# Optimization experiments

Hardware: AMD Instinct MI355X
Metric: run time of the kernel (lower is better)

## Reference

```python
import jax, jax.numpy as jnp
import numpy as np

DIM = 768
HEADS = 12
DIM_HEAD = 64
INNER = HEADS * DIM_HEAD  # 768
SCALE = DIM_HEAD ** -0.5
LN_EPS = 1e-5


def setup_inputs() -> dict:
    key = jax.random.key(0)
    ks = jax.random.split(key, 6)
    B, N = 2, 1024
    x = jax.random.normal(ks[0], (B, N, DIM), dtype=jnp.float32)
    ln_g = jnp.ones((DIM,), jnp.float32)
    ln_b = jnp.zeros((DIM,), jnp.float32)
    # torch nn.Linear weights are [out, in]
    w_qkv = jax.random.normal(ks[1], (3 * INNER, DIM), jnp.float32) * (DIM ** -0.5)
    w_out = jax.random.normal(ks[2], (DIM, INNER), jnp.float32) * (INNER ** -0.5)
    b_out = jnp.zeros((DIM,), jnp.float32)
    theta = jax.random.normal(ks[3], (HEADS, HEADS), jnp.float32)
    # xavier_uniform for 12x12
    lim = float(np.sqrt(6.0 / (HEADS + HEADS)))
    gnn_w = jax.random.uniform(ks[4], (HEADS, HEADS), jnp.float32, -lim, lim)
    return {"x": x, "ln_g": ln_g, "ln_b": ln_b, "w_qkv": w_qkv,
            "w_out": w_out, "b_out": b_out, "theta": theta, "gnn_w": gnn_w}


def _dc_crd(attn, theta, gnn_w):
    # attn: [B, H, N, N] treated as image with H=12 channels
    B, H, N, _ = attn.shape
    w = attn.mean(axis=(-2, -1))  # adaptive_avg_pool2d -> [B, H]
    diff = w[:, :, None] - w[:, None, :]  # [B, H, H]
    # abs(1 - exp(-d)/(1+exp(-d))) - 1 == abs(1 - sigmoid(-d)) - 1
    T_w = jnp.abs(1.0 - jax.nn.sigmoid(-diff)) - 1.0
    adj = (T_w + jnp.swapaxes(T_w, -1, -2)) * 0.5 * theta  # [B, H, H]
    attn_flat = attn.reshape(B, H, N * N)
    support = jnp.einsum('ij,bjm->bim', gnn_w, attn_flat)  # W @ features
    out = jax.nn.relu(jnp.einsum('bij,bjm->bim', adj, support))  # spmm(adj, support)
    return out.reshape(B, H, N, N)


def reference(x, ln_g, ln_b, w_qkv, w_out, b_out, theta, gnn_w):
    B, N, D = x.shape
    mu = x.mean(-1, keepdims=True)
    var = x.var(-1, keepdims=True)
    xn = (x - mu) * jax.lax.rsqrt(var + LN_EPS) * ln_g + ln_b
    qkv = xn @ w_qkv.T  # [B, N, 3*INNER]
    q, k, v = jnp.split(qkv, 3, axis=-1)
    def heads(t):
        return t.reshape(B, N, HEADS, DIM_HEAD).transpose(0, 2, 1, 3)
    q, k, v = heads(q), heads(k), heads(v)  # [B, H, N, d]
    dots = jnp.einsum('bhnd,bhmd->bhnm', q, k) * SCALE
    attn = jax.nn.softmax(dots, axis=-1)
    H = _dc_crd(attn, theta, gnn_w)
    out = jnp.einsum('bhnm,bhmd->bhnd', attn + H, v)
    out = out.transpose(0, 2, 1, 3).reshape(B, N, INNER)
    return out @ w_out.T + b_out
```

## Files before the change

kernel.cpp:

```cpp
#include <hip/hip_runtime.h>
#include <hip/hip_bf16.h>
#include <stdint.h>

#define NB 2
#define SEQ 1024
#define DMODEL 768
#define NH 12
#define DH 64
#define SCALE 0.125f
#define NCH 4

#define AJ_RS 1288
#define CT_HS 648

typedef __hip_bfloat16 bf16;
typedef __attribute__((ext_vector_type(8))) short short8;
typedef __attribute__((ext_vector_type(2))) short s2v;
typedef __attribute__((ext_vector_type(4))) float f32x4;

__device__ __forceinline__ bf16 f2b(float x){ return __float2bfloat16(x); }
__device__ __forceinline__ short f2bs(float x){
  bf16 h = __float2bfloat16(x); return *reinterpret_cast<short*>(&h);
}
__device__ __forceinline__ float s2f(short u){
  return __uint_as_float(((unsigned)(unsigned short)u) << 16);
}

__device__ __forceinline__ void gl_lds16(const bf16* g, bf16* l){
  __builtin_amdgcn_global_load_lds(
      (const __attribute__((address_space(1))) void*)g,
      (__attribute__((address_space(3))) void*)l, 16, 0, 0);
}

__global__ __launch_bounds__(256) void prep_all(const float* __restrict__ x,
                                                const float* __restrict__ g,
                                                const float* __restrict__ bta,
                                                const float* __restrict__ w1, int n1,
                                                const float* __restrict__ w2, int n2,
                                                const float* __restrict__ theta,
                                                const float* __restrict__ gnn,
                                                bf16* __restrict__ xn,
                                                bf16* __restrict__ wb,
                                                bf16* __restrict__ Mb,
                                                float* __restrict__ l){
  int bx = blockIdx.x, t = threadIdx.x;
  if (bx < 2048){
    const float* xr = x + (size_t)bx*DMODEL;
    float v0[3]; float s = 0.f, s2 = 0.f;
    #pragma unroll
    for (int i=0;i<3;i++){ float val = xr[t+256*i]; v0[i]=val; s+=val; s2+=val*val; }
    __shared__ float sb[256], s2b[256];
    sb[t]=s; s2b[t]=s2; __syncthreads();
    for (int off=128; off>0; off>>=1){
      if (t<off){ sb[t]+=sb[t+off]; s2b[t]+=s2b[t+off]; }
      __syncthreads();
    }
    float mean = sb[0]*(1.f/DMODEL);
    float var  = s2b[0]*(1.f/DMODEL) - mean*mean;
    float rstd = rsqrtf(var + 1e-5f);
    #pragma unroll
    for (int i=0;i<3;i++){
      int c = t+256*i;
      xn[(size_t)bx*DMODEL + c] = f2b((v0[i]-mean)*rstd*g[c] + bta[c]);
    }
  } else if (bx < 2048+9216){
    int i = (bx-2048)*256 + t;
    if (i < n1) wb[i] = f2b(w1[i]);
    else if (i < n1+n2) wb[i] = f2b(w2[i-n1]);
  } else {
    int sub = bx - (2048+9216);
    if (sub == 0){
      #pragma unroll
      for (int e=0;e<2;e++){
        int idx = t + 256*e;
        int i = idx >> 5, j = idx & 31;
        float sacc = 0.f;
        if (i < 12 && j < 12)
          for (int jj=0;jj<12;jj++) sacc += (-0.5f)*theta[i*12+jj] * gnn[jj*12+j];
        bf16 hi = f2b(sacc);
        float lo = sacc - __bfloat162float(hi);
        Mb[idx]       = hi;
        Mb[512 + idx] = f2b(lo);
      }
    } else {
      l[(sub-1)*256 + t] = 0.f;
    }
  }
}

__global__ __launch_bounds__(256) void gemm_qkv(const bf16* __restrict__ A,
                                                const bf16* __restrict__ W,
                                                bf16* __restrict__ q,
                                                bf16* __restrict__ k,
                                                bf16* __restrict__ vt){
  __shared__ bf16 As[128*32];
  __shared__ bf16 Bs[128*32];
  int n0 = blockIdx.x*128, m0 = blockIdx.y*128;
  int t = threadIdx.x, w = t>>6, lane = t&63;
  int ln16 = lane&15, q8 = (lane>>4)*8;
  int wm = w>>1, wn = w&1;
  f32x4 acc[4][4] = {};
  for (int k0=0; k0<768; k0+=32){
    __syncthreads();
    #pragma unroll
    for (int i=0;i<2;i++){
      int cc = t + i*256;
      int r = cc>>2, ko = (cc&3)*8;
      gl_lds16(&A[(size_t)(m0+r)*768 + k0+ko], &As[(size_t)(w*64 + i*256)*8]);
      gl_lds16(&W[(size_t)(n0+r)*768 + k0+ko], &Bs[(size_t)(w*64 + i*256)*8]);
    }
    __syncthreads();
    short8 af[4], bfr[4];
    #pragma unroll
    for (int mi=0;mi<4;mi++) af[mi]  = *(const short8*)&As[(wm*64+mi*16+ln16)*32 + q8];
    #pragma unroll
    for (int ni=0;ni<4;ni++) bfr[ni] = *(const short8*)&Bs[(wn*64+ni*16+ln16)*32 + q8];
    #pragma unroll
    for (int mi=0;mi<4;mi++)
      #pragma unroll
      for (int ni=0;ni<4;ni++)
        acc[mi][ni] = __builtin_amdgcn_mfma_f32_16x16x32_bf16(af[mi], bfr[ni], acc[mi][ni], 0, 0, 0);
  }
  int quad4 = (lane>>4)*4;
  #pragma unroll
  for (int mi=0;mi<4;mi++){
    #pragma unroll
    for (int ni=0;ni<4;ni++){
      int cg = n0 + wn*64 + ni*16 + ln16;
      int which = cg/768; int rem = cg - which*768;
      int h = rem>>6, dd = rem&63;
      #pragma unroll
      for (int r=0;r<4;r++){
        int m = m0 + wm*64 + mi*16 + quad4 + r;
        int bb = m>>10, n = m&1023;
        float val = acc[mi][ni][r];
        if (which==0)      q [((size_t)(bb*NH+h)*SEQ + n)*DH + dd] = f2b(val*SCALE);
        else if (which==1) k [((size_t)(bb*NH+h)*SEQ + n)*DH + dd] = f2b(val);
        else               vt[((size_t)(bb*NH+h)*DH + dd)*SEQ + n] = f2b(val);
      }
    }
  }
}

__global__ __launch_bounds__(768) void attn_sums(const bf16* __restrict__ q,
                                                 const bf16* __restrict__ k,
                                                 float* __restrict__ l){
  int b = blockIdx.z, ch = blockIdx.y; int r0 = blockIdx.x*16;
  int t = threadIdx.x; int h = t>>6; int lane = t&63;
  int ln16 = lane&15, quad = lane>>4; int q8 = quad*8, quad4 = quad*4;
  const bf16* qrow = q + ((size_t)(b*NH+h)*SEQ + r0 + ln16)*DH;
  short8 aq0 = *(const short8*)(qrow + q8);
  short8 aq1 = *(const short8*)(qrow + 32 + q8);
  const bf16* kB = k + ((size_t)(b*NH+h)*SEQ)*DH;
  float ls[4] = {0.f,0.f,0.f,0.f};
  #pragma unroll 4
  for (int i=0;i<16;i++){
    int c0 = ch*256 + i*16;
    const bf16* krow = kB + (size_t)(c0 + ln16)*DH;
    short8 bk0 = *(const short8*)(krow + q8);
    short8 bk1 = *(const short8*)(krow + 32 + q8);
    f32x4 a = {0.f,0.f,0.f,0.f};
    a = __builtin_amdgcn_mfma_f32_16x16x32_bf16(aq0, bk0, a, 0, 0, 0);
    a = __builtin_amdgcn_mfma_f32_16x16x32_bf16(aq1, bk1, a, 0, 0, 0);
    #pragma unroll
    for (int r=0;r<4;r++) ls[r] += __expf(a[r]);
  }
  #pragma unroll
  for (int msk=1; msk<16; msk<<=1){
    #pragma unroll
    for (int r=0;r<4;r++) ls[r] += __shfl_xor(ls[r], msk);
  }
  if (ln16 == 0){
    #pragma unroll
    for (int r=0;r<4;r++)
      atomicAdd(&l[((size_t)(b*NH+h))*SEQ + r0 + quad4 + r], ls[r]);
  }
}

__global__ __launch_bounds__(768) void attn_main(const bf16* __restrict__ q,
                                                 const bf16* __restrict__ k,
                                                 const bf16* __restrict__ vt,
                                                 const bf16* __restrict__ Mb,
                                                 const float* __restrict__ l,
                                                 bf16* __restrict__ opart){
  __shared__ __align__(16) bf16 attJ[16*AJ_RS];
  __shared__ __align__(16) bf16 combT[16*CT_HS];
  int b = blockIdx.z, ch = blockIdx.y; int r0 = blockIdx.x*16;
  int t = threadIdx.x; int h = t>>6; int lane = t&63;
  int ln16 = lane&15, quad = lane>>4; int q8 = quad*8, quad4 = quad*4;
  const bf16* kB = k  + ((size_t)(b*NH+h)*SEQ)*DH;
  const bf16* vB = vt + ((size_t)(b*NH+h)*DH)*SEQ;

  short8 z8 = (short8){0,0,0,0,0,0,0,0};
  for (int i = t*8; i < 16*AJ_RS; i += 768*8) *(short8*)&attJ[i] = z8;

  short8 mhi = *(const short8*)&Mb[ln16*32 + q8];
  short8 mlo = *(const short8*)&Mb[512 + ln16*32 + q8];

  const bf16* qrow = q + ((size_t)(b*NH+h)*SEQ + r0 + ln16)*DH;
  short8 aq0 = *(const short8*)(qrow + q8);
  short8 aq1 = *(const short8*)(qrow + 32 + q8);

  float inv_l[4];
  #pragma unroll
  for (int r=0;r<4;r++) inv_l[r] = 1.0f / l[((size_t)(b*NH+h))*SEQ + r0 + quad4 + r];

  __syncthreads();

  f32x4 oacc[4] = {};
  for (int it=0; it<8; it++){
    int c0 = ch*256 + it*32;
    #pragma unroll
    for (int half=0; half<2; half++){
      const bf16* krow = kB + (size_t)(c0 + half*16 + ln16)*DH;
      short8 bk0 = *(const short8*)(krow + q8);
      short8 bk1 = *(const short8*)(krow + 32 + q8);
      f32x4 a = {0.f,0.f,0.f,0.f};
      a = __builtin_amdgcn_mfma_f32_16x16x32_bf16(aq0, bk0, a, 0, 0, 0);
      a = __builtin_amdgcn_mfma_f32_16x16x32_bf16(aq1, bk1, a, 0, 0, 0);
      int cc = half*16 + ln16;
      #pragma unroll
      for (int r=0;r<4;r++)
        attJ[(quad4+r)*AJ_RS + cc*40 + h] = f2b(__expf(a[r])*inv_l[r]);
    }
    __syncthreads();
    for (int tl = h; tl < 32; tl += 12){
      int n = tl*16 + ln16;
      int base = (n>>5)*AJ_RS + (n&31)*40;
      short8 bfrag = *(const short8*)&attJ[base + q8];
      f32x4 c = {0.f,0.f,0.f,0.f};
      c = __builtin_amdgcn_mfma_f32_16x16x32_bf16(mlo, bfrag, c, 0, 0, 0);
      c = __builtin_amdgcn_mfma_f32_16x16x32_bf16(mhi, bfrag, c, 0, 0, 0);
      s2v id01 = *(const s2v*)&attJ[base + quad4];
      s2v id23 = *(const s2v*)&attJ[base + quad4 + 2];
      float idf[4] = { s2f(id01[0]), s2f(id01[1]), s2f(id23[0]), s2f(id23[1]) };
      int cbase = (n>>5)*40 + (n&31);
      #pragma unroll
      for (int ri=0; ri<4; ri++)
        combT[(quad4+ri)*CT_HS + cbase] = f2b(idf[ri] + fmaxf(c[ri], 0.f));
    }
    __syncthreads();
    short8 afrag = *(const short8*)&combT[h*CT_HS + ln16*40 + q8];
    #pragma unroll
    for (int ni=0; ni<4; ni++){
      short8 bv = *(const short8*)&vB[(size_t)(ni*16 + ln16)*SEQ + c0 + q8];
      oacc[ni] = __builtin_amdgcn_mfma_f32_16x16x32_bf16(afrag, bv, oacc[ni], 0, 0, 0);
    }
  }
  bf16* dst = opart + ((size_t)ch*NB*SEQ + (size_t)b*SEQ)*DMODEL;
  #pragma unroll
  for (int ni=0; ni<4; ni++)
    #pragma unroll
    for (int r=0; r<4; r++){
      int n = r0 + quad4 + r;
      dst[(size_t)n*DMODEL + h*DH + ni*16 + ln16] = f2b(oacc[ni][r]);
    }
}

__global__ __launch_bounds__(256) void reduce_kernel(const bf16* __restrict__ opart,
                                                     bf16* __restrict__ aout){
  const size_t TOT = (size_t)NB*SEQ*DMODEL;
  size_t i = ((size_t)blockIdx.x*256 + threadIdx.x)*8;
  float s[8] = {};
  #pragma unroll
  for (int c=0;c<NCH;c++){
    short8 u = *(const short8*)&opart[c*TOT + i];
    #pragma unroll
    for (int e=0;e<8;e++) s[e] += s2f(u[e]);
  }
  short8 o;
  #pragma unroll
  for (int e=0;e<8;e++) o[e] = f2bs(s[e]);
  *(short8*)&aout[i] = o;
}

__global__ __launch_bounds__(256) void gemm_out(const bf16* __restrict__ A,
                                                const bf16* __restrict__ W,
                                                const float* __restrict__ bias,
                                                float* __restrict__ out){
  __shared__ bf16 As[64*32];
  __shared__ bf16 Bs[64*32];
  int n0 = blockIdx.x*64, m0 = blockIdx.y*64;
  int t = threadIdx.x, w = t>>6, lane = t&63;
  int ln16 = lane&15, q8 = (lane>>4)*8;
  int wm = w>>1, wn = w&1;
  f32x4 acc[2][2] = {};
  for (int k0=0; k0<768; k0+=32){
    __syncthreads();
    {
      int r = t>>2, ko = (t&3)*8;
      gl_lds16(&A[(size_t)(m0+r)*768 + k0+ko], &As[(size_t)(w*64)*8]);
      gl_lds16(&W[(size_t)(n0+r)*768 + k0+ko], &Bs[(size_t)(w*64)*8]);
    }
    __syncthreads();
    short8 af[2], bfr[2];
    #pragma unroll
    for (int mi=0;mi<2;mi++) af[mi]  = *(const short8*)&As[(wm*32+mi*16+ln16)*32 + q8];
    #pragma unroll
    for (int ni=0;ni<2;ni++) bfr[ni] = *(const short8*)&Bs[(wn*32+ni*16+ln16)*32 + q8];
    #pragma unroll
    for (int mi=0;mi<2;mi++)
      #pragma unroll
      for (int ni=0;ni<2;ni++)
        acc[mi][ni] = __builtin_amdgcn_mfma_f32_16x16x32_bf16(af[mi], bfr[ni], acc[mi][ni], 0, 0, 0);
  }
  int quad4 = (lane>>4)*4;
  #pragma unroll
  for (int mi=0;mi<2;mi++)
    #pragma unroll
    for (int ni=0;ni<2;ni++){
      int cg = n0 + wn*32 + ni*16 + ln16;
      #pragma unroll
      for (int r=0;r<4;r++){
        int m = m0 + wm*32 + mi*16 + quad4 + r;
        out[(size_t)m*768 + cg] = acc[mi][ni][r] + bias[cg];
      }
    }
}

extern "C" void kernel_launch(void* const* d_in, const int* in_sizes, int n_in,
                              void* d_out, int out_size, void* d_ws, size_t ws_size,
                              hipStream_t stream){
  const float* x     = (const float*)d_in[0];
  const float* ln_g  = (const float*)d_in[1];
  const float* ln_b  = (const float*)d_in[2];
  const float* w_qkv = (const float*)d_in[3];
  const float* w_out = (const float*)d_in[4];
  const float* b_out = (const float*)d_in[5];
  const float* theta = (const float*)d_in[6];
  const float* gnn   = (const float*)d_in[7];
  float* out = (float*)d_out;

  char* p = (char*)d_ws;
  bf16* xnb   = (bf16*)p; p += (size_t)2048*768*2;
  bf16* wqkvb = (bf16*)p; p += (size_t)2304*768*2;
  bf16* woutb = (bf16*)p; p += (size_t)768*768*2;
  bf16* qb    = (bf16*)p; p += (size_t)NB*NH*SEQ*DH*2;
  bf16* kb    = (bf16*)p; p += (size_t)NB*NH*SEQ*DH*2;
  bf16* vtb   = (bf16*)p; p += (size_t)NB*NH*SEQ*DH*2;
  bf16* aoutb = (bf16*)p; p += (size_t)2048*768*2;
  bf16* Mbw   = (bf16*)p; p += (size_t)1024*2;
  float* lsum = (float*)p; p += (size_t)NB*NH*SEQ*4;
  bf16* opart = (bf16*)p;

  const int N1 = 2304*768, N2 = 768*768;
  prep_all<<<dim3(2048+9216+97), dim3(256), 0, stream>>>(
      x, ln_g, ln_b, w_qkv, N1, w_out, N2, theta, gnn, xnb, wqkvb, Mbw, lsum);
  gemm_qkv<<<dim3(18, 16), dim3(256), 0, stream>>>(xnb, wqkvb, qb, kb, vtb);
  attn_sums<<<dim3(64, NCH, NB), dim3(768), 0, stream>>>(qb, kb, lsum);
  attn_main<<<dim3(64, NCH, NB), dim3(768), 0, stream>>>(qb, kb, vtb, Mbw, lsum, opart);
  reduce_kernel<<<dim3(NB*SEQ*DMODEL/(8*256)), dim3(256), 0, stream>>>(opart, aoutb);
  gemm_out<<<dim3(12, 32), dim3(256), 0, stream>>>(aoutb, woutb, b_out, out);
}
```

Measured before the change: 202.0 us.

## Fuse attention row-sum and main attention kernels with inter-block spin barrier

Merges the softmax-denominator kernel and the main attention kernel into one launch. Each block computes its partial row sums, atomically adds them, then spins on a per-row-block counter until all NCH column-chunk blocks have contributed, and reads the totals back through atomics. This removes one kernel launch and keeps the Q fragments and setup in registers across both phases. It relies on all four chunk blocks of a row group being co-resident, which risks deadlock or stalls, and the spin-wait adds latency.

```diff
diff --git a/kernel.cpp b/kernel.cpp
--- a/kernel.cpp
+++ b/kernel.cpp
@@ -42,7 +42,8 @@
                                                 bf16* __restrict__ xn,
                                                 bf16* __restrict__ wb,
                                                 bf16* __restrict__ Mb,
-                                                float* __restrict__ l){
+                                                float* __restrict__ l,
+                                                unsigned* __restrict__ cnt){
   int bx = blockIdx.x, t = threadIdx.x;
   if (bx < 2048){
     const float* xr = x + (size_t)bx*DMODEL;
@@ -82,8 +83,10 @@
         Mb[idx]       = hi;
         Mb[512 + idx] = f2b(lo);
       }
+    } else if (sub <= 96){
+      l[(sub-1)*256 + t] = 0.f;
     } else {
-      l[(sub-1)*256 + t] = 0.f;
+      if (t < 128) cnt[t] = 0u;
     }
   }
 }
@@ -142,16 +145,31 @@
   }
 }
 
-__global__ __launch_bounds__(768) void attn_sums(const bf16* __restrict__ q,
-                                                 const bf16* __restrict__ k,
-                                                 float* __restrict__ l){
+__global__ __launch_bounds__(768) void attn_fused(const bf16* __restrict__ q,
+                                                  const bf16* __restrict__ k,
+                                                  const bf16* __restrict__ vt,
+                                                  const bf16* __restrict__ Mb,
+                                                  float* __restrict__ l,
+                                                  unsigned* __restrict__ cnt,
+                                                  bf16* __restrict__ opart){
+  __shared__ __align__(16) bf16 attJ[16*AJ_RS];
+  __shared__ __align__(16) bf16 combT[16*CT_HS];
   int b = blockIdx.z, ch = blockIdx.y; int r0 = blockIdx.x*16;
   int t = threadIdx.x; int h = t>>6; int lane = t&63;
   int ln16 = lane&15, quad = lane>>4; int q8 = quad*8, quad4 = quad*4;
+  const bf16* kB = k  + ((size_t)(b*NH+h)*SEQ)*DH;
+  const bf16* vB = vt + ((size_t)(b*NH+h)*DH)*SEQ;
+
+  short8 z8 = (short8){0,0,0,0,0,0,0,0};
+  for (int i = t*8; i < 16*AJ_RS; i += 768*8) *(short8*)&attJ[i] = z8;
+
+  short8 mhi = *(const short8*)&Mb[ln16*32 + q8];
+  short8 mlo = *(const short8*)&Mb[512 + ln16*32 + q8];
+
   const bf16* qrow = q + ((size_t)(b*NH+h)*SEQ + r0 + ln16)*DH;
   short8 aq0 = *(const short8*)(qrow + q8);
   short8 aq1 = *(const short8*)(qrow + 32 + q8);
-  const bf16* kB = k + ((size_t)(b*NH+h)*SEQ)*DH;
+
   float ls[4] = {0.f,0.f,0.f,0.f};
   #pragma unroll 4
   for (int i=0;i<16;i++){
@@ -170,42 +188,27 @@
     #pragma unroll
     for (int r=0;r<4;r++) ls[r] += __shfl_xor(ls[r], msk);
   }
+  size_t lbase = ((size_t)(b*NH+h))*SEQ + r0 + quad4;
   if (ln16 == 0){
     #pragma unroll
-    for (int r=0;r<4;r++)
-      atomicAdd(&l[((size_t)(b*NH+h))*SEQ + r0 + quad4 + r], ls[r]);
-  }
-}
-
-__global__ __launch_bounds__(768) void attn_main(const bf16* __restrict__ q,
-                                                 const bf16* __restrict__ k,
-                                                 const bf16* __restrict__ vt,
-                                                 const bf16* __restrict__ Mb,
-                                                 const float* __restrict__ l,
-                                                 bf16* __restrict__ opart){
-  __shared__ __align__(16) bf16 attJ[16*AJ_RS];
-  __shared__ __align__(16) bf16 combT[16*CT_HS];
-  int b = blockIdx.z, ch = blockIdx.y; int r0 = blockIdx.x*16;
-  int t = threadIdx.x; int h = t>>6; int lane = t&63;
-  int ln16 = lane&15, quad = lane>>4; int q8 = quad*8, quad4 = quad*4;
-  const bf16* kB = k  + ((size_t)(b*NH+h)*SEQ)*DH;
-  const bf16* vB = vt + ((size_t)(b*NH+h)*DH)*SEQ;
-
-  short8 z8 = (short8){0,0,0,0,0,0,0,0};
-  for (int i = t*8; i < 16*AJ_RS; i += 768*8) *(short8*)&attJ[i] = z8;
-
-  short8 mhi = *(const short8*)&Mb[ln16*32 + q8];
-  short8 mlo = *(const short8*)&Mb[512 + ln16*32 + q8];
-
-  const bf16* qrow = q + ((size_t)(b*NH+h)*SEQ + r0 + ln16)*DH;
-  short8 aq0 = *(const short8*)(qrow + q8);
-  short8 aq1 = *(const short8*)(qrow + 32 + q8);
-
+    for (int r=0;r<4;r++) atomicAdd(&l[lbase + r], ls[r]);
+  }
+
+  __threadfence();
+  __syncthreads();
+  int gidx = b*64 + blockIdx.x;
+  if (t == 0){
+    atomicAdd(&cnt[gidx], 1u);
+    while (atomicAdd(&cnt[gidx], 0u) < NCH) __builtin_amdgcn_s_sleep(2);
+  }
+  __syncthreads();
+
+  float lv[4];
+  #pragma unroll
+  for (int r=0;r<4;r++) lv[r] = (ln16 == 0) ? atomicAdd(&l[lbase + r], 0.0f) : 0.f;
   float inv_l[4];
   #pragma unroll
-  for (int r=0;r<4;r++) inv_l[r] = 1.0f / l[((size_t)(b*NH+h))*SEQ + r0 + quad4 + r];
-
-  __syncthreads();
+  for (int r=0;r<4;r++) inv_l[r] = 1.0f / __shfl(lv[r], quad*16);
 
   f32x4 oacc[4] = {};
   for (int it=0; it<8; it++){
@@ -285,13 +288,11 @@
   int ln16 = lane&15, q8 = (lane>>4)*8;
   int wm = w>>1, wn = w&1;
   f32x4 acc[2][2] = {};
+  int r = t>>2, ko = (t&3)*8;
   for (int k0=0; k0<768; k0+=32){
     __syncthreads();
-    {
-      int r = t>>2, ko = (t&3)*8;
-      gl_lds16(&A[(size_t)(m0+r)*768 + k0+ko], &As[(size_t)(w*64)*8]);
-      gl_lds16(&W[(size_t)(n0+r)*768 + k0+ko], &Bs[(size_t)(w*64)*8]);
-    }
+    gl_lds16(&A[(size_t)(m0+r)*768 + k0+ko], &As[(size_t)(w*64)*8]);
+    gl_lds16(&W[(size_t)(n0+r)*768 + k0+ko], &Bs[(size_t)(w*64)*8]);
     __syncthreads();
     short8 af[2], bfr[2];
     #pragma unroll
@@ -311,9 +312,9 @@
     for (int ni=0;ni<2;ni++){
       int cg = n0 + wn*32 + ni*16 + ln16;
       #pragma unroll
-      for (int r=0;r<4;r++){
-        int m = m0 + wm*32 + mi*16 + quad4 + r;
-        out[(size_t)m*768 + cg] = acc[mi][ni][r] + bias[cg];
+      for (int rr=0;rr<4;rr++){
+        int m = m0 + wm*32 + mi*16 + quad4 + rr;
+        out[(size_t)m*768 + cg] = acc[mi][ni][rr] + bias[cg];
       }
     }
 }
@@ -341,14 +342,14 @@
   bf16* aoutb = (bf16*)p; p += (size_t)2048*768*2;
   bf16* Mbw   = (bf16*)p; p += (size_t)1024*2;
   float* lsum = (float*)p; p += (size_t)NB*NH*SEQ*4;
+  unsigned* cntw = (unsigned*)p; p += (size_t)128*4;
   bf16* opart = (bf16*)p;
 
   const int N1 = 2304*768, N2 = 768*768;
-  prep_all<<<dim3(2048+9216+97), dim3(256), 0, stream>>>(
-      x, ln_g, ln_b, w_qkv, N1, w_out, N2, theta, gnn, xnb, wqkvb, Mbw, lsum);
+  prep_all<<<dim3(2048+9216+98), dim3(256), 0, stream>>>(
+      x, ln_g, ln_b, w_qkv, N1, w_out, N2, theta, gnn, xnb, wqkvb, Mbw, lsum, cntw);
   gemm_qkv<<<dim3(18, 16), dim3(256), 0, stream>>>(xnb, wqkvb, qb, kb, vtb);
-  attn_sums<<<dim3(64, NCH, NB), dim3(768), 0, stream>>>(qb, kb, lsum);
-  attn_main<<<dim3(64, NCH, NB), dim3(768), 0, stream>>>(qb, kb, vtb, Mbw, lsum, opart);
+  attn_fused<<<dim3(64, NCH, NB), dim3(768), 0, stream>>>(qb, kb, vtb, Mbw, lsum, cntw, opart);
   reduce_kernel<<<dim3(NB*SEQ*DMODEL/(8*256)), dim3(256), 0, stream>>>(opart, aoutb);
   gemm_out<<<dim3(12, 32), dim3(256), 0, stream>>>(aoutb, woutb, b_out, out);
 }
```

Result: slower. 319.7 us (+58.3%).

## Store unnormalized exp scores in attn_sums, reuse in attn_main, fuse reduce into gemm_out

Applied to the files above, without the earlier changes.

attn_sums now writes the bf16 exp(QK) values it computes to a workspace buffer. attn_main reads them back, prefetching the next iteration, instead of recomputing the QK MFMAs and exps. The separate reduce kernel is removed: gemm_out sums the NCH partial outputs while loading its A tile. This trades recomputation for about 50MB of extra global traffic (NB*NH*SEQ*SEQ*2 bytes written and read), and it adds an extra bf16 rounding before normalization.

```diff
diff --git a/kernel.cpp b/kernel.cpp
--- a/kernel.cpp
+++ b/kernel.cpp
@@ -17,6 +17,7 @@
 typedef __attribute__((ext_vector_type(8))) short short8;
 typedef __attribute__((ext_vector_type(2))) short s2v;
 typedef __attribute__((ext_vector_type(4))) float f32x4;
+typedef unsigned long long u64;
 
 __device__ __forceinline__ bf16 f2b(float x){ return __float2bfloat16(x); }
 __device__ __forceinline__ short f2bs(float x){
@@ -144,14 +145,16 @@
 
 __global__ __launch_bounds__(768) void attn_sums(const bf16* __restrict__ q,
                                                  const bf16* __restrict__ k,
-                                                 float* __restrict__ l){
-  int b = blockIdx.z, ch = blockIdx.y; int r0 = blockIdx.x*16;
+                                                 float* __restrict__ l,
+                                                 u64* __restrict__ pst){
+  int rg = blockIdx.x, ch = blockIdx.y, b = blockIdx.z; int r0 = rg*16;
   int t = threadIdx.x; int h = t>>6; int lane = t&63;
   int ln16 = lane&15, quad = lane>>4; int q8 = quad*8, quad4 = quad*4;
   const bf16* qrow = q + ((size_t)(b*NH+h)*SEQ + r0 + ln16)*DH;
   short8 aq0 = *(const short8*)(qrow + q8);
   short8 aq1 = *(const short8*)(qrow + 32 + q8);
   const bf16* kB = k + ((size_t)(b*NH+h)*SEQ)*DH;
+  u64* pb = pst + ((((size_t)(b*NCH+ch)*64 + rg)*NH + h)*16)*64 + lane;
   float ls[4] = {0.f,0.f,0.f,0.f};
   #pragma unroll 4
   for (int i=0;i<16;i++){
@@ -162,8 +165,11 @@
     f32x4 a = {0.f,0.f,0.f,0.f};
     a = __builtin_amdgcn_mfma_f32_16x16x32_bf16(aq0, bk0, a, 0, 0, 0);
     a = __builtin_amdgcn_mfma_f32_16x16x32_bf16(aq1, bk1, a, 0, 0, 0);
-    #pragma unroll
-    for (int r=0;r<4;r++) ls[r] += __expf(a[r]);
+    float e0 = __expf(a[0]), e1 = __expf(a[1]), e2 = __expf(a[2]), e3 = __expf(a[3]);
+    ls[0]+=e0; ls[1]+=e1; ls[2]+=e2; ls[3]+=e3;
+    unsigned p0 = ((unsigned)(unsigned short)f2bs(e1) << 16) | (unsigned)(unsigned short)f2bs(e0);
+    unsigned p1 = ((unsigned)(unsigned short)f2bs(e3) << 16) | (unsigned)(unsigned short)f2bs(e2);
+    pb[(size_t)i*64] = ((u64)p1 << 32) | (u64)p0;
   }
   #pragma unroll
   for (int msk=1; msk<16; msk<<=1){
@@ -177,19 +183,18 @@
   }
 }
 
-__global__ __launch_bounds__(768) void attn_main(const bf16* __restrict__ q,
-                                                 const bf16* __restrict__ k,
-                                                 const bf16* __restrict__ vt,
-                                                 const bf16* __restrict__ Mb,
-                                                 const float* __restrict__ l,
-                                                 bf16* __restrict__ opart){
+__global__ __launch_bounds__(768, 6) void attn_main(const bf16* __restrict__ vt,
+                                                    const bf16* __restrict__ Mb,
+                                                    const float* __restrict__ l,
+                                                    const u64* __restrict__ pst,
+                                                    bf16* __restrict__ opart){
   __shared__ __align__(16) bf16 attJ[16*AJ_RS];
   __shared__ __align__(16) bf16 combT[16*CT_HS];
-  int b = blockIdx.z, ch = blockIdx.y; int r0 = blockIdx.x*16;
+  int rg = blockIdx.x, ch = blockIdx.y, b = blockIdx.z; int r0 = rg*16;
   int t = threadIdx.x; int h = t>>6; int lane = t&63;
   int ln16 = lane&15, quad = lane>>4; int q8 = quad*8, quad4 = quad*4;
-  const bf16* kB = k  + ((size_t)(b*NH+h)*SEQ)*DH;
   const bf16* vB = vt + ((size_t)(b*NH+h)*DH)*SEQ;
+  const u64* pb = pst + ((((size_t)(b*NCH+ch)*64 + rg)*NH + h)*16)*64 + lane;
 
   short8 z8 = (short8){0,0,0,0,0,0,0,0};
   for (int i = t*8; i < 16*AJ_RS; i += 768*8) *(short8*)&attJ[i] = z8;
@@ -197,31 +202,28 @@
   short8 mhi = *(const short8*)&Mb[ln16*32 + q8];
   short8 mlo = *(const short8*)&Mb[512 + ln16*32 + q8];
 
-  const bf16* qrow = q + ((size_t)(b*NH+h)*SEQ + r0 + ln16)*DH;
-  short8 aq0 = *(const short8*)(qrow + q8);
-  short8 aq1 = *(const short8*)(qrow + 32 + q8);
-
   float inv_l[4];
   #pragma unroll
   for (int r=0;r<4;r++) inv_l[r] = 1.0f / l[((size_t)(b*NH+h))*SEQ + r0 + quad4 + r];
+
+  u64 cur0 = pb[0*64], cur1 = pb[1*64];
 
   __syncthreads();
 
   f32x4 oacc[4] = {};
   for (int it=0; it<8; it++){
     int c0 = ch*256 + it*32;
+    int nx = (it+1)&7;
+    u64 n0 = pb[(size_t)(nx*2+0)*64], n1 = pb[(size_t)(nx*2+1)*64];
     #pragma unroll
     for (int half=0; half<2; half++){
-      const bf16* krow = kB + (size_t)(c0 + half*16 + ln16)*DH;
-      short8 bk0 = *(const short8*)(krow + q8);
-      short8 bk1 = *(const short8*)(krow + 32 + q8);
-      f32x4 a = {0.f,0.f,0.f,0.f};
-      a = __builtin_amdgcn_mfma_f32_16x16x32_bf16(aq0, bk0, a, 0, 0, 0);
-      a = __builtin_amdgcn_mfma_f32_16x16x32_bf16(aq1, bk1, a, 0, 0, 0);
       int cc = half*16 + ln16;
-      #pragma unroll
-      for (int r=0;r<4;r++)
-        attJ[(quad4+r)*AJ_RS + cc*40 + h] = f2b(__expf(a[r])*inv_l[r]);
+      u64 cu = half ? cur1 : cur0;
+      unsigned p0 = (unsigned)cu, p1 = (unsigned)(cu >> 32);
+      attJ[(quad4+0)*AJ_RS + cc*40 + h] = f2b(s2f((short)(p0 & 0xffff))*inv_l[0]);
+      attJ[(quad4+1)*AJ_RS + cc*40 + h] = f2b(s2f((short)(p0 >> 16))   *inv_l[1]);
+      attJ[(quad4+2)*AJ_RS + cc*40 + h] = f2b(s2f((short)(p1 & 0xffff))*inv_l[2]);
+      attJ[(quad4+3)*AJ_RS + cc*40 + h] = f2b(s2f((short)(p1 >> 16))   *inv_l[3]);
     }
     __syncthreads();
     for (int tl = h; tl < 32; tl += 12){
@@ -246,6 +248,7 @@
       short8 bv = *(const short8*)&vB[(size_t)(ni*16 + ln16)*SEQ + c0 + q8];
       oacc[ni] = __builtin_amdgcn_mfma_f32_16x16x32_bf16(afrag, bv, oacc[ni], 0, 0, 0);
     }
+    cur0 = n0; cur1 = n1;
   }
   bf16* dst = opart + ((size_t)ch*NB*SEQ + (size_t)b*SEQ)*DMODEL;
   #pragma unroll
@@ -257,41 +260,33 @@
     }
 }
 
-__global__ __launch_bounds__(256) void reduce_kernel(const bf16* __restrict__ opart,
-                                                     bf16* __restrict__ aout){
-  const size_t TOT = (size_t)NB*SEQ*DMODEL;
-  size_t i = ((size_t)blockIdx.x*256 + threadIdx.x)*8;
-  float s[8] = {};
-  #pragma unroll
-  for (int c=0;c<NCH;c++){
-    short8 u = *(const short8*)&opart[c*TOT + i];
-    #pragma unroll
-    for (int e=0;e<8;e++) s[e] += s2f(u[e]);
-  }
-  short8 o;
-  #pragma unroll
-  for (int e=0;e<8;e++) o[e] = f2bs(s[e]);
-  *(short8*)&aout[i] = o;
-}
-
-__global__ __launch_bounds__(256) void gemm_out(const bf16* __restrict__ A,
+__global__ __launch_bounds__(256) void gemm_out(const bf16* __restrict__ opart,
                                                 const bf16* __restrict__ W,
                                                 const float* __restrict__ bias,
                                                 float* __restrict__ out){
   __shared__ bf16 As[64*32];
   __shared__ bf16 Bs[64*32];
+  const size_t TOT = (size_t)NB*SEQ*DMODEL;
   int n0 = blockIdx.x*64, m0 = blockIdx.y*64;
   int t = threadIdx.x, w = t>>6, lane = t&63;
   int ln16 = lane&15, q8 = (lane>>4)*8;
   int wm = w>>1, wn = w&1;
   f32x4 acc[2][2] = {};
+  int r = t>>2, ko = (t&3)*8;
   for (int k0=0; k0<768; k0+=32){
     __syncthreads();
-    {
-      int r = t>>2, ko = (t&3)*8;
-      gl_lds16(&A[(size_t)(m0+r)*768 + k0+ko], &As[(size_t)(w*64)*8]);
-      gl_lds16(&W[(size_t)(n0+r)*768 + k0+ko], &Bs[(size_t)(w*64)*8]);
-    }
+    gl_lds16(&W[(size_t)(n0+r)*768 + k0+ko], &Bs[(size_t)(w*64)*8]);
+    float s[8] = {};
+    #pragma unroll
+    for (int c=0;c<NCH;c++){
+      short8 u = *(const short8*)&opart[(size_t)c*TOT + (size_t)(m0+r)*768 + k0+ko];
+      #pragma unroll
+      for (int e=0;e<8;e++) s[e] += s2f(u[e]);
+    }
+    short8 o8;
+    #pragma unroll
+    for (int e=0;e<8;e++) o8[e] = f2bs(s[e]);
+    *(short8*)&As[r*32 + ko] = o8;
     __syncthreads();
     short8 af[2], bfr[2];
     #pragma unroll
@@ -311,9 +306,9 @@
     for (int ni=0;ni<2;ni++){
       int cg = n0 + wn*32 + ni*16 + ln16;
       #pragma unroll
-      for (int r=0;r<4;r++){
-        int m = m0 + wm*32 + mi*16 + quad4 + r;
-        out[(size_t)m*768 + cg] = acc[mi][ni][r] + bias[cg];
+      for (int rr=0;rr<4;rr++){
+        int m = m0 + wm*32 + mi*16 + quad4 + rr;
+        out[(size_t)m*768 + cg] = acc[mi][ni][rr] + bias[cg];
       }
     }
 }
@@ -338,17 +333,16 @@
   bf16* qb    = (bf16*)p; p += (size_t)NB*NH*SEQ*DH*2;
   bf16* kb    = (bf16*)p; p += (size_t)NB*NH*SEQ*DH*2;
   bf16* vtb   = (bf16*)p; p += (size_t)NB*NH*SEQ*DH*2;
-  bf16* aoutb = (bf16*)p; p += (size_t)2048*768*2;
   bf16* Mbw   = (bf16*)p; p += (size_t)1024*2;
   float* lsum = (float*)p; p += (size_t)NB*NH*SEQ*4;
-  bf16* opart = (bf16*)p;
+  bf16* opart = (bf16*)p; p += (size_t)NCH*NB*SEQ*DMODEL*2;
+  u64*  pstw  = (u64*)p;
 
   const int N1 = 2304*768, N2 = 768*768;
   prep_all<<<dim3(2048+9216+97), dim3(256), 0, stream>>>(
       x, ln_g, ln_b, w_qkv, N1, w_out, N2, theta, gnn, xnb, wqkvb, Mbw, lsum);
   gemm_qkv<<<dim3(18, 16), dim3(256), 0, stream>>>(xnb, wqkvb, qb, kb, vtb);
-  attn_sums<<<dim3(64, NCH, NB), dim3(768), 0, stream>>>(qb, kb, lsum);
-  attn_main<<<dim3(64, NCH, NB), dim3(768), 0, stream>>>(qb, kb, vtb, Mbw, lsum, opart);
-  reduce_kernel<<<dim3(NB*SEQ*DMODEL/(8*256)), dim3(256), 0, stream>>>(opart, aoutb);
-  gemm_out<<<dim3(12, 32), dim3(256), 0, stream>>>(aoutb, woutb, b_out, out);
-}
+  attn_sums<<<dim3(64, NCH, NB), dim3(768), 0, stream>>>(qb, kb, lsum, pstw);
+  attn_main<<<dim3(64, NCH, NB), dim3(768), 0, stream>>>(vtb, Mbw, lsum, pstw, opart);
+  gemm_out<<<dim3(12, 32), dim3(256), 0, stream>>>(opart, woutb, b_out, out);
+}
```

Measured after the change: 198.3 us. Within noise of the previous version (-1.8%).
